# Optimization experiments

Measured on AMD Instinct MI355X. Metric: run time of the kernel, lower is better.

Reference implementation:

```python
import jax, jax.numpy as jnp
import numpy as np

N = 100000      # nodes
E = 3200000     # edges (avg degree 32)
F_IN = 512
F_OUT = 512


def setup_inputs() -> dict:
    key = jax.random.key(0)
    k1, k2, k3, k4 = jax.random.split(key, 4)
    x = jax.random.normal(k1, (N, F_IN), dtype=jnp.float32)
    edge_index = jax.random.randint(k2, (2, E), 0, N, dtype=jnp.int64)
    edge_weight = jax.random.uniform(k3, (E,), dtype=jnp.float32)
    weight = jax.random.normal(k4, (F_IN, F_OUT), dtype=jnp.float32) * (1.0 / np.sqrt(F_IN))
    bias = jnp.ones((F_OUT,), dtype=jnp.float32)
    return {"x": x, "edge_index": edge_index, "edge_weight": edge_weight,
            "weight": weight, "bias": bias}


def reference(x, edge_index, edge_weight, weight, bias):
    # support = X @ W  -> [N, F_OUT]
    support = x @ weight
    # SpMM: out[r] = sum_{edges e with row r} w_e * support[col_e]
    row, col = edge_index[0], edge_index[1]
    msg = support[col] * edge_weight[:, None]            # [E, F_OUT]
    out = jax.ops.segment_sum(msg, row, num_segments=N)  # [N, F_OUT]
    return out + bias
```

## Files before the change

kernel.cpp:

```cpp
#include <hip/hip_runtime.h>
#include <hip/hip_bf16.h>
#include <cstdint>

#define NNODES 100000
#define NEDGES 3200000
#define FDIM   512
#define MPAD   100096

typedef __bf16 bf16_t;
typedef __bf16 bf16x8 __attribute__((ext_vector_type(8)));
typedef float  f32x4  __attribute__((ext_vector_type(4)));

static __device__ __forceinline__ bf16x8 ld_frag(const ushort* p) {
    return __builtin_bit_cast(bf16x8, *(const uint4*)p);
}


__global__ void cast_x_kernel(const float* __restrict__ x, ushort* __restrict__ xb) {
    size_t t = (size_t)blockIdx.x * 256 + threadIdx.x;
    size_t base = t * 4;
    int row = (int)(base >> 9);
    ushort4 pk;
    if (row < NNODES) {
        float4 v = *(const float4*)(x + base);
        pk.x = __builtin_bit_cast(ushort, (bf16_t)v.x);
        pk.y = __builtin_bit_cast(ushort, (bf16_t)v.y);
        pk.z = __builtin_bit_cast(ushort, (bf16_t)v.z);
        pk.w = __builtin_bit_cast(ushort, (bf16_t)v.w);
    } else {
        pk.x = pk.y = pk.z = pk.w = 0;
    }
    *(ushort4*)(xb + base) = pk;
}

__global__ void cast_wt_kernel(const float* __restrict__ w, ushort* __restrict__ wt) {
    int t = blockIdx.x * 256 + threadIdx.x;
    int n = t >> 9, k = t & 511;
    wt[(size_t)n * 512 + k] = __builtin_bit_cast(ushort, (bf16_t)w[(size_t)k * 512 + n]);
}

__global__ __launch_bounds__(256) void gemm_kernel(const ushort* __restrict__ xb,
                                                   const ushort* __restrict__ wt,
                                                   ushort* __restrict__ sup) {
    __shared__ ushort As[4 * 128 * 8];
    __shared__ ushort Bs[4 * 128 * 8];

    const int tid  = threadIdx.x;
    const int m0   = blockIdx.y * 128;
    const int n0   = blockIdx.x * 128;
    const int wave = tid >> 6, lane = tid & 63;
    const int quad = lane >> 4, r16 = lane & 15;
    const int wm = (wave >> 1) * 64, wn = (wave & 1) * 64;

    const int qa = tid >> 7, ra = tid & 127;

    f32x4 acc[4][4];
#pragma unroll
    for (int i = 0; i < 4; ++i)
#pragma unroll
        for (int j = 0; j < 4; ++j) acc[i][j] = f32x4{0.f, 0.f, 0.f, 0.f};

    const size_t arow = (size_t)(m0 + ra) * 512;
    const size_t brow = (size_t)(n0 + ra) * 512;

    for (int kc = 0; kc < 16; ++kc) {
        const int k0 = kc * 32;
        __syncthreads();
        *(uint4*)(As + ((qa    ) * 128 + ra) * 8) = *(const uint4*)(xb + arow + k0 + (qa    ) * 8);
        *(uint4*)(As + ((qa + 2) * 128 + ra) * 8) = *(const uint4*)(xb + arow + k0 + (qa + 2) * 8);
        *(uint4*)(Bs + ((qa    ) * 128 + ra) * 8) = *(const uint4*)(wt + brow + k0 + (qa    ) * 8);
        *(uint4*)(Bs + ((qa + 2) * 128 + ra) * 8) = *(const uint4*)(wt + brow + k0 + (qa + 2) * 8);
        __syncthreads();

        bf16x8 af[4], bfr[4];
#pragma unroll
        for (int i = 0; i < 4; ++i) af[i]  = ld_frag(As + (quad * 128 + wm + 16 * i + r16) * 8);
#pragma unroll
        for (int j = 0; j < 4; ++j) bfr[j] = ld_frag(Bs + (quad * 128 + wn + 16 * j + r16) * 8);

#pragma unroll
        for (int i = 0; i < 4; ++i)
#pragma unroll
            for (int j = 0; j < 4; ++j)
                acc[i][j] = __builtin_amdgcn_mfma_f32_16x16x32_bf16(af[i], bfr[j], acc[i][j], 0, 0, 0);
    }

#pragma unroll
    for (int i = 0; i < 4; ++i) {
        const int rowb = m0 + wm + 16 * i + quad * 4;
#pragma unroll
        for (int j = 0; j < 4; ++j) {
            const int col = n0 + wn + 16 * j + r16;
            f32x4 v = acc[i][j];
#pragma unroll
            for (int r = 0; r < 4; ++r)
                sup[(size_t)(rowb + r) * 512 + col] = __builtin_bit_cast(ushort, (bf16_t)v[r]);
        }
    }
}


__global__ void zero_cnt_kernel(int* __restrict__ cnt, int* __restrict__ fill) {
    int i = blockIdx.x * 256 + threadIdx.x;
    if (i < NNODES) { cnt[i] = 0; fill[i] = 0; }
}

__global__ void hist_kernel(const int* __restrict__ ei, int* __restrict__ cnt) {
    int e = blockIdx.x * 256 + threadIdx.x;
    if (e < NEDGES) atomicAdd(&cnt[ei[e]], 1);
}

__global__ __launch_bounds__(1024) void scan_kernel(const int* __restrict__ cnt, int* __restrict__ ptr) {
    __shared__ int sums[1024];
    const int t = threadIdx.x;
    const int CH = (NNODES + 1023) / 1024;
    const int b = t * CH;
    const int e = min(b + CH, NNODES);
    int s = 0;
    for (int i = b; i < e; ++i) s += cnt[i];
    sums[t] = s;
    __syncthreads();
    for (int off = 1; off < 1024; off <<= 1) {
        int v = (t >= off) ? sums[t - off] : 0;
        __syncthreads();
        sums[t] += v;
        __syncthreads();
    }
    int run = sums[t] - s;
    for (int i = b; i < e; ++i) { ptr[i] = run; run += cnt[i]; }
    if (t == 0) ptr[NNODES] = NEDGES;
}

__global__ void scatter_kernel(const int* __restrict__ ei, const float* __restrict__ ew,
                               const int* __restrict__ ptr, int* __restrict__ fill,
                               int* __restrict__ cols, float* __restrict__ wsrt) {
    int e = blockIdx.x * 256 + threadIdx.x;
    if (e < NEDGES) {
        int r = ei[e];
        int pos = ptr[r] + atomicAdd(&fill[r], 1);
        cols[pos] = ei[NEDGES + e];
        wsrt[pos] = ew[e];
    }
}

__global__ __launch_bounds__(256) void spmm_kernel(const ushort* __restrict__ sup,
                                                   const int* __restrict__ ptr,
                                                   const int* __restrict__ cols,
                                                   const float* __restrict__ wsrt,
                                                   const float* __restrict__ bias,
                                                   float* __restrict__ out) {
    const int row  = blockIdx.x * 4 + (threadIdx.x >> 6);
    const int lane = threadIdx.x & 63;
    const int fo   = lane * 8;
    const int start = ptr[row], end = ptr[row + 1];

    float acc[8];
#pragma unroll
    for (int j = 0; j < 8; ++j) acc[j] = 0.f;

    int i = start;
    for (; i + 4 <= end; i += 4) {
        const int   c0 = cols[i],     c1 = cols[i + 1], c2 = cols[i + 2], c3 = cols[i + 3];
        const float w0 = wsrt[i],     w1 = wsrt[i + 1], w2 = wsrt[i + 2], w3 = wsrt[i + 3];
        const bf16x8 s0 = __builtin_bit_cast(bf16x8, *(const uint4*)(sup + (size_t)c0 * 512 + fo));
        const bf16x8 s1 = __builtin_bit_cast(bf16x8, *(const uint4*)(sup + (size_t)c1 * 512 + fo));
        const bf16x8 s2 = __builtin_bit_cast(bf16x8, *(const uint4*)(sup + (size_t)c2 * 512 + fo));
        const bf16x8 s3 = __builtin_bit_cast(bf16x8, *(const uint4*)(sup + (size_t)c3 * 512 + fo));
#pragma unroll
        for (int j = 0; j < 8; ++j) {
            acc[j] += w0 * (float)s0[j];
            acc[j] += w1 * (float)s1[j];
            acc[j] += w2 * (float)s2[j];
            acc[j] += w3 * (float)s3[j];
        }
    }
    for (; i < end; ++i) {
        const int c = cols[i];
        const float w = wsrt[i];
        bf16x8 sv = __builtin_bit_cast(bf16x8, *(const uint4*)(sup + (size_t)c * 512 + fo));
#pragma unroll
        for (int j = 0; j < 8; ++j) acc[j] += w * (float)sv[j];
    }

    const float4 b0 = *(const float4*)(bias + fo);
    const float4 b1 = *(const float4*)(bias + fo + 4);
    float* op = out + (size_t)row * 512 + fo;
    *(float4*)(op)     = make_float4(acc[0] + b0.x, acc[1] + b0.y, acc[2] + b0.z, acc[3] + b0.w);
    *(float4*)(op + 4) = make_float4(acc[4] + b1.x, acc[5] + b1.y, acc[6] + b1.z, acc[7] + b1.w);
}


extern "C" void kernel_launch(void* const* d_in, const int* in_sizes, int n_in,
                              void* d_out, int out_size, void* d_ws, size_t ws_size,
                              hipStream_t stream) {
    const float* x    = (const float*)d_in[0];
    const int*   ei   = (const int*)d_in[1];
    const float* ew   = (const float*)d_in[2];
    const float* w    = (const float*)d_in[3];
    const float* bias = (const float*)d_in[4];
    float* out = (float*)d_out;

    char* ws = (char*)d_ws;
    size_t off = 0;
    auto take = [&](size_t bytes) { char* p = ws + off; off = (off + bytes + 255) & ~(size_t)255; return p; };

    ushort* xb   = (ushort*)take((size_t)MPAD * FDIM * 2);
    ushort* sup  = (ushort*)take((size_t)MPAD * FDIM * 2);
    ushort* wt   = (ushort*)take((size_t)FDIM * FDIM * 2);
    int*   cnt   = (int*)take((size_t)NNODES * 4);
    int*   ptr   = (int*)take((size_t)(NNODES + 1) * 4);
    int*   fill  = (int*)take((size_t)NNODES * 4);
    int*   cols  = (int*)take((size_t)NEDGES * 4);
    float* wsrt  = (float*)take((size_t)NEDGES * 4);

    hipLaunchKernelGGL(cast_x_kernel, dim3((MPAD * FDIM / 4) / 256), dim3(256), 0, stream, x, xb);
    hipLaunchKernelGGL(cast_wt_kernel, dim3(1024), dim3(256), 0, stream, w, wt);
    hipLaunchKernelGGL(gemm_kernel, dim3(FDIM / 128, MPAD / 128), dim3(256), 0, stream, xb, wt, sup);
    hipLaunchKernelGGL(zero_cnt_kernel, dim3((NNODES + 255) / 256), dim3(256), 0, stream, cnt, fill);
    hipLaunchKernelGGL(hist_kernel, dim3(NEDGES / 256), dim3(256), 0, stream, ei, cnt);
    hipLaunchKernelGGL(scan_kernel, dim3(1), dim3(1024), 0, stream, cnt, ptr);
    hipLaunchKernelGGL(scatter_kernel, dim3(NEDGES / 256), dim3(256), 0, stream, ei, ew, ptr, fill, cols, wsrt);
    hipLaunchKernelGGL(spmm_kernel, dim3(NNODES / 4), dim3(256), 0, stream, sup, ptr, cols, wsrt, bias, out);
}
```

Baseline: 1.405 ms.

## Split support matrix into feature halves for cache-local SpMM gather; async LDS loads

The GEMM now writes the support matrix as two column halves, each a contiguous MPAD x 256 bf16 slab. The SpMM launches a second grid dimension so each half is gathered separately, which shrinks the random-gather working set per pass to about half and should fit caches better. Each lane reads 4 bf16 values instead of 8, and the output uses nontemporal stores. The GEMM tile loads switch to global_load_lds direct-to-LDS copies. The cost is twice the CSR index and weight reads and smaller per-lane loads.

```diff
diff --git a/kernel.cpp b/kernel.cpp
--- a/kernel.cpp
+++ b/kernel.cpp
@@ -5,14 +5,23 @@
 #define NNODES 100000
 #define NEDGES 3200000
 #define FDIM   512
+#define FHALF  256
 #define MPAD   100096
 
 typedef __bf16 bf16_t;
 typedef __bf16 bf16x8 __attribute__((ext_vector_type(8)));
+typedef __bf16 bf16x4 __attribute__((ext_vector_type(4)));
 typedef float  f32x4  __attribute__((ext_vector_type(4)));
 
 static __device__ __forceinline__ bf16x8 ld_frag(const ushort* p) {
     return __builtin_bit_cast(bf16x8, *(const uint4*)p);
+}
+
+typedef __attribute__((address_space(3))) ushort as3_ushort;
+typedef __attribute__((address_space(1))) const ushort as1_ushort;
+static __device__ __forceinline__ void gl_lds16(const ushort* g, ushort* l) {
+    __builtin_amdgcn_global_load_lds((as1_ushort*)(uintptr_t)g,
+                                     (as3_ushort*)(uintptr_t)l, 16, 0, 0);
 }
 
 
@@ -66,10 +75,10 @@
     for (int kc = 0; kc < 16; ++kc) {
         const int k0 = kc * 32;
         __syncthreads();
-        *(uint4*)(As + ((qa    ) * 128 + ra) * 8) = *(const uint4*)(xb + arow + k0 + (qa    ) * 8);
-        *(uint4*)(As + ((qa + 2) * 128 + ra) * 8) = *(const uint4*)(xb + arow + k0 + (qa + 2) * 8);
-        *(uint4*)(Bs + ((qa    ) * 128 + ra) * 8) = *(const uint4*)(wt + brow + k0 + (qa    ) * 8);
-        *(uint4*)(Bs + ((qa + 2) * 128 + ra) * 8) = *(const uint4*)(wt + brow + k0 + (qa + 2) * 8);
+        gl_lds16(xb + arow + k0 + (qa    ) * 8, As + (size_t)tid * 8);
+        gl_lds16(xb + arow + k0 + (qa + 2) * 8, As + (size_t)(tid + 256) * 8);
+        gl_lds16(wt + brow + k0 + (qa    ) * 8, Bs + (size_t)tid * 8);
+        gl_lds16(wt + brow + k0 + (qa + 2) * 8, Bs + (size_t)(tid + 256) * 8);
         __syncthreads();
 
         bf16x8 af[4], bfr[4];
@@ -91,10 +100,11 @@
 #pragma unroll
         for (int j = 0; j < 4; ++j) {
             const int col = n0 + wn + 16 * j + r16;
+            const size_t base = (size_t)(col >> 8) * MPAD * FHALF + (col & 255);
             f32x4 v = acc[i][j];
 #pragma unroll
             for (int r = 0; r < 4; ++r)
-                sup[(size_t)(rowb + r) * 512 + col] = __builtin_bit_cast(ushort, (bf16_t)v[r]);
+                sup[base + (size_t)(rowb + r) * FHALF] = __builtin_bit_cast(ushort, (bf16_t)v[r]);
         }
     }
 }
@@ -150,24 +160,26 @@
                                                    const float* __restrict__ bias,
                                                    float* __restrict__ out) {
     const int row  = blockIdx.x * 4 + (threadIdx.x >> 6);
+    const int half = blockIdx.y;
+    const ushort* suph = sup + (size_t)half * MPAD * FHALF;
     const int lane = threadIdx.x & 63;
-    const int fo   = lane * 8;
+    const int fo   = lane * 4;
     const int start = ptr[row], end = ptr[row + 1];
 
-    float acc[8];
-#pragma unroll
-    for (int j = 0; j < 8; ++j) acc[j] = 0.f;
+    float acc[4];
+#pragma unroll
+    for (int j = 0; j < 4; ++j) acc[j] = 0.f;
 
     int i = start;
     for (; i + 4 <= end; i += 4) {
         const int   c0 = cols[i],     c1 = cols[i + 1], c2 = cols[i + 2], c3 = cols[i + 3];
         const float w0 = wsrt[i],     w1 = wsrt[i + 1], w2 = wsrt[i + 2], w3 = wsrt[i + 3];
-        const bf16x8 s0 = __builtin_bit_cast(bf16x8, *(const uint4*)(sup + (size_t)c0 * 512 + fo));
-        const bf16x8 s1 = __builtin_bit_cast(bf16x8, *(const uint4*)(sup + (size_t)c1 * 512 + fo));
-        const bf16x8 s2 = __builtin_bit_cast(bf16x8, *(const uint4*)(sup + (size_t)c2 * 512 + fo));
-        const bf16x8 s3 = __builtin_bit_cast(bf16x8, *(const uint4*)(sup + (size_t)c3 * 512 + fo));
-#pragma unroll
-        for (int j = 0; j < 8; ++j) {
+        const bf16x4 s0 = __builtin_bit_cast(bf16x4, *(const uint2*)(suph + (size_t)c0 * FHALF + fo));
+        const bf16x4 s1 = __builtin_bit_cast(bf16x4, *(const uint2*)(suph + (size_t)c1 * FHALF + fo));
+        const bf16x4 s2 = __builtin_bit_cast(bf16x4, *(const uint2*)(suph + (size_t)c2 * FHALF + fo));
+        const bf16x4 s3 = __builtin_bit_cast(bf16x4, *(const uint2*)(suph + (size_t)c3 * FHALF + fo));
+#pragma unroll
+        for (int j = 0; j < 4; ++j) {
             acc[j] += w0 * (float)s0[j];
             acc[j] += w1 * (float)s1[j];
             acc[j] += w2 * (float)s2[j];
@@ -177,16 +189,16 @@
     for (; i < end; ++i) {
         const int c = cols[i];
         const float w = wsrt[i];
-        bf16x8 sv = __builtin_bit_cast(bf16x8, *(const uint4*)(sup + (size_t)c * 512 + fo));
-#pragma unroll
-        for (int j = 0; j < 8; ++j) acc[j] += w * (float)sv[j];
-    }
-
-    const float4 b0 = *(const float4*)(bias + fo);
-    const float4 b1 = *(const float4*)(bias + fo + 4);
-    float* op = out + (size_t)row * 512 + fo;
-    *(float4*)(op)     = make_float4(acc[0] + b0.x, acc[1] + b0.y, acc[2] + b0.z, acc[3] + b0.w);
-    *(float4*)(op + 4) = make_float4(acc[4] + b1.x, acc[5] + b1.y, acc[6] + b1.z, acc[7] + b1.w);
+        const bf16x4 sv = __builtin_bit_cast(bf16x4, *(const uint2*)(suph + (size_t)c * FHALF + fo));
+#pragma unroll
+        for (int j = 0; j < 4; ++j) acc[j] += w * (float)sv[j];
+    }
+
+    const int fglob = half * FHALF + fo;
+    const float4 b0 = *(const float4*)(bias + fglob);
+    f32x4 o;
+    o[0] = acc[0] + b0.x; o[1] = acc[1] + b0.y; o[2] = acc[2] + b0.z; o[3] = acc[3] + b0.w;
+    __builtin_nontemporal_store(o, (f32x4*)(out + (size_t)row * 512 + fglob));
 }
 
 
@@ -220,5 +232,5 @@
     hipLaunchKernelGGL(hist_kernel, dim3(NEDGES / 256), dim3(256), 0, stream, ei, cnt);
     hipLaunchKernelGGL(scan_kernel, dim3(1), dim3(1024), 0, stream, cnt, ptr);
     hipLaunchKernelGGL(scatter_kernel, dim3(NEDGES / 256), dim3(256), 0, stream, ei, ew, ptr, fill, cols, wsrt);
-    hipLaunchKernelGGL(spmm_kernel, dim3(NNODES / 4), dim3(256), 0, stream, sup, ptr, cols, wsrt, bias, out);
-}
+    hipLaunchKernelGGL(spmm_kernel, dim3(NNODES / 4, 2), dim3(256), 0, stream, sup, ptr, cols, wsrt, bias, out);
+}
```

Result: faster. 1.377 ms (-2.0%).
